# Optimization experiments

Measured on AMD Instinct MI355X. Metric: run time of the kernel, lower is better.

Reference implementation:

```python
import jax, jax.numpy as jnp
import numpy as np
import math

B, L, D, K = 8, 8192, 256, 2
J = math.ceil(math.log((L - 1) / (K - 1) + 1) / math.log(K))  # 13 for L=8192, K=2


def setup_inputs() -> dict:
    key = jax.random.key(0)
    kx, k0, k1, kw = jax.random.split(key, 4)
    # matches nn.initializers.normal(stddev=h_scale) in the flax module
    h_scale = math.sqrt((math.gamma(K / 2) / math.gamma(J + K / 2)) ** (1.0 / J) / 2.0)
    x = jax.random.normal(kx, (B, L, D), dtype=jnp.float32)
    h0 = jax.random.normal(k0, (D, K), dtype=jnp.float32) * h_scale
    h1 = jax.random.normal(k1, (D, K), dtype=jnp.float32) * h_scale
    w = jax.random.normal(kw, (J + 2, D), dtype=jnp.float32) / math.sqrt(J + 2)
    return {"x": x, "h0": h0, "h1": h1, "w": w}


def _depthwise_conv(a, filt, dilation, d):
    # a: (B, L', D), filt: (1, D, K) in IOL layout, depthwise via feature_group_count=D
    return jax.lax.conv_general_dilated(
        lhs=a, rhs=filt, window_strides=(1,), padding='VALID',
        dimension_numbers=('NLC', 'IOL', 'NLC'),
        rhs_dilation=(dilation,), feature_group_count=d)


def reference(x, h0, h1, w):
    Kf = h0.shape[-1]
    Dd = x.shape[-1]
    h0r = h0[None, :, :]  # (1, D, K)
    h1r = h1[None, :, :]
    Jlv = w.shape[0] - 2
    y = jnp.zeros_like(x)
    a = x
    for j in range(Jlv):
        dilation = Kf ** j
        pad = dilation * (Kf - 1)
        a = jnp.pad(a, ((0, 0), (pad, 0), (0, 0)))  # pad left (pad_right=False)
        b = _depthwise_conv(a, h1r, dilation, Dd)
        a = _depthwise_conv(a, h0r, dilation, Dd)
        y = y + w[j + 1][None, None, :] * b
    y = y + w[None, :1, :] * x + w[None, -1:, :] * a
    return y
```

## Files before the change

kernel.cpp:

```cpp
#include <hip/hip_runtime.h>
#include <hip/hip_bf16.h>
#include <stdint.h>

namespace {

constexpr int L = 8192;
constexpr int D = 256;

constexpr int K1_CT  = 32;
constexpr int K1_OUT = 192;
constexpr int K1_S   = 265;

constexpr int K2_CT = 32;
constexpr int K2_T2 = 2;
constexpr int K2_S  = 131;

__device__ __forceinline__ int phi1(int p) { return p + (p >> 5); }
__device__ __forceinline__ int phi2(int t) { return t + (t >> 5); }

__device__ __forceinline__ uint32_t pk2(float ylo, float ahi) {
    union { __hip_bfloat16 h; uint16_t u; } a, b;
    a.h = __float2bfloat16(ylo);
    b.h = __float2bfloat16(ahi);
    return ((uint32_t)b.u << 16) | (uint32_t)a.u;
}
__device__ __forceinline__ float up_lo(uint32_t u) { return __uint_as_float(u << 16); }
__device__ __forceinline__ float up_hi(uint32_t u) { return __uint_as_float(u & 0xffff0000u); }

__device__ __forceinline__ void lvl4(float (&a)[4], float (&y)[4],
                                     float l0, float l1, float l2, float l3,
                                     float h00, float h01, float h10, float h11,
                                     float wj) {
    const float lk[4] = {l0, l1, l2, l3};
#pragma unroll
    for (int i = 0; i < 4; ++i) {
        const float bv = lk[i] * h10 + a[i] * h11;
        y[i] = fmaf(wj, bv, y[i]);
        a[i] = lk[i] * h00 + a[i] * h01;
    }
}

__device__ __forceinline__ void lvl2f(float& a0, float& a1, float& y0, float& y1,
                                      float l0, float l1,
                                      float h00, float h01, float h10, float h11,
                                      float wj) {
    const float bv0 = l0 * h10 + a0 * h11;
    const float bv1 = l1 * h10 + a1 * h11;
    y0 = fmaf(wj, bv0, y0);
    y1 = fmaf(wj, bv1, y1);
    a0 = l0 * h00 + a0 * h01;
    a1 = l1 * h00 + a1 * h01;
}

__global__ __launch_bounds__(512, 8)
void mrl_k1(const float* __restrict__ x, const float* __restrict__ h0,
            const float* __restrict__ h1, const float* __restrict__ w,
            uint32_t* __restrict__ out_pk) {
    __shared__ uint32_t lds[K1_CT * K1_S];
    __shared__ float cf[11 * K1_CT];
    const int tid = threadIdx.x;
    const int b  = blockIdx.z;
    const int c0 = blockIdx.y * K1_CT;
    const int t0 = blockIdx.x * K1_OUT;
    const int tsb = t0 - 64;

    if (tid < 11 * K1_CT) {
        const int r = tid >> 5, i = tid & 31;
        float v;
        if (r < 7)       v = w[r * D + c0 + i];
        else if (r == 7) v = h0[2 * (c0 + i)];
        else if (r == 8) v = h0[2 * (c0 + i) + 1];
        else if (r == 9) v = h1[2 * (c0 + i)];
        else             v = h1[2 * (c0 + i) + 1];
        cf[tid] = v;
    }

    {
        const int cq = (tid & 7) * 4;
        const int tr = tid >> 3;
        const float* xb = x + (size_t)b * L * D + c0 + cq;
#pragma unroll
        for (int it = 0; it < 4; ++it) {
            const int p = it * 64 + tr;
            const int t = tsb + p;
            float4 v = make_float4(0.f, 0.f, 0.f, 0.f);
            if (t >= 0 && t < L) v = *reinterpret_cast<const float4*>(xb + (size_t)t * D);
            const int ph = phi1(p);
            lds[(cq + 0) * K1_S + ph] = __float_as_uint(v.x);
            lds[(cq + 1) * K1_S + ph] = __float_as_uint(v.y);
            lds[(cq + 2) * K1_S + ph] = __float_as_uint(v.z);
            lds[(cq + 3) * K1_S + ph] = __float_as_uint(v.w);
        }
    }
    __syncthreads();

    {
        const int lane = tid & 63;
        const int wv   = tid >> 6;
        const int p0   = 4 * lane;
#pragma unroll
        for (int q = 0; q < 4; ++q) {
            const int cl = wv + 8 * q;
            const float h00 = cf[7*K1_CT + cl], h01 = cf[8*K1_CT + cl];
            const float h10 = cf[9*K1_CT + cl], h11 = cf[10*K1_CT + cl];
            const int base = cl * K1_S;
            float a[4], y[4];
            {
                const float w0 = cf[cl];
#pragma unroll
                for (int i = 0; i < 4; ++i) {
                    a[i] = __uint_as_float(lds[base + phi1(p0 + i)]);
                    y[i] = w0 * a[i];
                }
            }
            lvl4(a, y, __shfl_up(a[3], 1), a[0], a[1], a[2],
                 h00, h01, h10, h11, cf[1*K1_CT + cl]);
            lvl4(a, y, __shfl_up(a[2], 1), __shfl_up(a[3], 1), a[0], a[1],
                 h00, h01, h10, h11, cf[2*K1_CT + cl]);
            lvl4(a, y, __shfl_up(a[0], 1), __shfl_up(a[1], 1),
                       __shfl_up(a[2], 1), __shfl_up(a[3], 1),
                 h00, h01, h10, h11, cf[3*K1_CT + cl]);
            lvl4(a, y, __shfl_up(a[0], 2), __shfl_up(a[1], 2),
                       __shfl_up(a[2], 2), __shfl_up(a[3], 2),
                 h00, h01, h10, h11, cf[4*K1_CT + cl]);
            lvl4(a, y, __shfl_up(a[0], 4), __shfl_up(a[1], 4),
                       __shfl_up(a[2], 4), __shfl_up(a[3], 4),
                 h00, h01, h10, h11, cf[5*K1_CT + cl]);
            lvl4(a, y, __shfl_up(a[0], 8), __shfl_up(a[1], 8),
                       __shfl_up(a[2], 8), __shfl_up(a[3], 8),
                 h00, h01, h10, h11, cf[6*K1_CT + cl]);
#pragma unroll
            for (int i = 0; i < 4; ++i)
                lds[base + phi1(p0 + i)] = pk2(y[i], a[i]);
        }
    }
    __syncthreads();

    {
        const int cq = (tid & 7) * 4;
        const int tr = tid >> 3;
        uint32_t* ob = out_pk + (size_t)b * L * D + c0 + cq;
#pragma unroll
        for (int it = 0; it < 3; ++it) {
            const int p = 64 + it * 64 + tr;
            const int t = tsb + p;
            if (t < L) {
                const int ph = phi1(p);
                uint4 v;
                v.x = lds[(cq + 0) * K1_S + ph];
                v.y = lds[(cq + 1) * K1_S + ph];
                v.z = lds[(cq + 2) * K1_S + ph];
                v.w = lds[(cq + 3) * K1_S + ph];
                *reinterpret_cast<uint4*>(ob + (size_t)t * D) = v;
            }
        }
    }
}

__global__ __launch_bounds__(512, 8)
void mrl_k2(const float* __restrict__ h0, const float* __restrict__ h1,
            const float* __restrict__ w, float* __restrict__ y) {
    __shared__ uint32_t lds[K2_CT * K2_T2 * K2_S];
    __shared__ float cf[12 * K2_CT];
    const int tid = threadIdx.x;
    const int b   = blockIdx.z;
    const int c0  = blockIdx.y * K2_CT;
    const int t2a = blockIdx.x * K2_T2;
    uint32_t* yb = reinterpret_cast<uint32_t*>(y) + (size_t)b * L * D + c0;

    if (tid < 12 * K2_CT) {
        const int r = tid >> 5, i = tid & 31;
        float v;
        if (r < 8)        v = w[(r + 7) * D + c0 + i];
        else if (r == 8)  v = h0[2 * (c0 + i)];
        else if (r == 9)  v = h0[2 * (c0 + i) + 1];
        else if (r == 10) v = h1[2 * (c0 + i)];
        else              v = h1[2 * (c0 + i) + 1];
        cf[tid] = v;
    }

    {
        const int cq  = (tid & 7) * 4;
        const int t2i = (tid >> 3) & 1;
        const int t1r = tid >> 4;
#pragma unroll
        for (int it = 0; it < 4; ++it) {
            const int t1 = it * 32 + t1r;
            const int t  = t1 * 64 + t2a + t2i;
            const uint4 v = *reinterpret_cast<const uint4*>(yb + (size_t)t * D + cq);
            const int ph = phi2(t1);
            lds[((cq + 0) * 2 + t2i) * K2_S + ph] = v.x;
            lds[((cq + 1) * 2 + t2i) * K2_S + ph] = v.y;
            lds[((cq + 2) * 2 + t2i) * K2_S + ph] = v.z;
            lds[((cq + 3) * 2 + t2i) * K2_S + ph] = v.w;
        }
    }
    __syncthreads();

    {
        const int lane = tid & 63;
        const int wv   = tid >> 6;
#pragma unroll
        for (int q = 0; q < 8; ++q) {
            const int pr = wv + 8 * q;
            const int cl = pr >> 1;
            const float h00 = cf[8*K2_CT + cl],  h01 = cf[9*K2_CT + cl];
            const float h10 = cf[10*K2_CT + cl], h11 = cf[11*K2_CT + cl];
            const int base = pr * K2_S;
            float a0, a1, y0, y1v;
            {
                const uint32_t u0 = lds[base + phi2(2 * lane)];
                const uint32_t u1 = lds[base + phi2(2 * lane + 1)];
                a0 = up_hi(u0); y0  = up_lo(u0);
                a1 = up_hi(u1); y1v = up_lo(u1);
            }
            {
                const float s = __shfl_up(a1, 1);
                const float l0 = (lane >= 1) ? s : 0.f;
                lvl2f(a0, a1, y0, y1v, l0, a0, h00, h01, h10, h11, cf[cl]);
            }
#pragma unroll
            for (int k = 0; k < 6; ++k) {
                const int m = 1 << k;
                const float wj = cf[(1 + k) * K2_CT + cl];
                const float s0 = __shfl_up(a0, m);
                const float s1 = __shfl_up(a1, m);
                const bool ok = (lane >= m);
                const float l0 = ok ? s0 : 0.f;
                const float l1 = ok ? s1 : 0.f;
                lvl2f(a0, a1, y0, y1v, l0, l1, h00, h01, h10, h11, wj);
            }
            const float w14 = cf[7 * K2_CT + cl];
            y0  = fmaf(w14, a0, y0);
            y1v = fmaf(w14, a1, y1v);
            lds[base + phi2(2 * lane)]     = __float_as_uint(y0);
            lds[base + phi2(2 * lane + 1)] = __float_as_uint(y1v);
        }
    }
    __syncthreads();

    {
        const int cq = (tid & 7) * 4;
        const int rq = tid >> 3;
#pragma unroll
        for (int it = 0; it < 4; ++it) {
            const int row = it * 64 + rq;
            const int t1 = row >> 1, t2i = row & 1;
            const int t  = t1 * 64 + t2a + t2i;
            const int ph = phi2(t1);
            uint4 v;
            v.x = lds[((cq + 0) * 2 + t2i) * K2_S + ph];
            v.y = lds[((cq + 1) * 2 + t2i) * K2_S + ph];
            v.z = lds[((cq + 2) * 2 + t2i) * K2_S + ph];
            v.w = lds[((cq + 3) * 2 + t2i) * K2_S + ph];
            *reinterpret_cast<uint4*>(yb + (size_t)t * D + cq) = v;
        }
    }
}

}

extern "C" void kernel_launch(void* const* d_in, const int* in_sizes, int n_in,
                              void* d_out, int out_size, void* d_ws, size_t ws_size,
                              hipStream_t stream) {
    const float* x  = (const float*)d_in[0];
    const float* h0 = (const float*)d_in[1];
    const float* h1 = (const float*)d_in[2];
    const float* w  = (const float*)d_in[3];
    float* y = (float*)d_out;
    (void)d_ws; (void)ws_size;

    const int B = in_sizes[0] / (L * D);

    dim3 g1((L + K1_OUT - 1) / K1_OUT, D / K1_CT, B);
    dim3 g2(64 / K2_T2, D / K2_CT, B);

    mrl_k1<<<g1, 512, 0, stream>>>(x, h0, h1, w, (uint32_t*)y);
    mrl_k2<<<g2, 512, 0, stream>>>(h0, h1, w, y);
}
```

Measured before the change: 164.7 us.

## Interleave channel chains, vectorize LDS accesses, load coefficients as scalars

Both kernels now process all of a wave's channels level by level instead of one channel at a time. The independent shuffle and FMA chains can then overlap and hide cross-lane latency. The LDS padding changes from one to two words per 32 elements, so each thread's 4 or 2 consecutive values can be read and written with 64-bit LDS accesses. The shared coefficient table and its staging are removed; filter and weight values are loaded directly from global memory using wave-uniform (readfirstlane) channel indices. The cost is higher register pressure from holding all per-channel state at once, which could limit occupancy or cause spills.

```diff
diff --git a/kernel.cpp b/kernel.cpp
--- a/kernel.cpp
+++ b/kernel.cpp
@@ -9,14 +9,13 @@
 
 constexpr int K1_CT  = 32;
 constexpr int K1_OUT = 192;
-constexpr int K1_S   = 265;
+constexpr int K1_S   = 270;
 
 constexpr int K2_CT = 32;
 constexpr int K2_T2 = 2;
-constexpr int K2_S  = 131;
-
-__device__ __forceinline__ int phi1(int p) { return p + (p >> 5); }
-__device__ __forceinline__ int phi2(int t) { return t + (t >> 5); }
+constexpr int K2_S  = 134;
+
+__device__ __forceinline__ int phie(int p) { return p + 2 * (p >> 5); }
 
 __device__ __forceinline__ uint32_t pk2(float ylo, float ahi) {
     union { __hip_bfloat16 h; uint16_t u; } a, b;
@@ -27,6 +26,12 @@
 __device__ __forceinline__ float up_lo(uint32_t u) { return __uint_as_float(u << 16); }
 __device__ __forceinline__ float up_hi(uint32_t u) { return __uint_as_float(u & 0xffff0000u); }
 
+__device__ __forceinline__ float sh1(float v) { return __shfl_up(v, 1); }
+__device__ __forceinline__ float sh1z(float v, int lane) {
+    const float s = __shfl_up(v, 1);
+    return (lane >= 1) ? s : 0.f;
+}
+
 __device__ __forceinline__ void lvl4(float (&a)[4], float (&y)[4],
                                      float l0, float l1, float l2, float l3,
                                      float h00, float h01, float h10, float h11,
@@ -40,41 +45,17 @@
     }
 }
 
-__device__ __forceinline__ void lvl2f(float& a0, float& a1, float& y0, float& y1,
-                                      float l0, float l1,
-                                      float h00, float h01, float h10, float h11,
-                                      float wj) {
-    const float bv0 = l0 * h10 + a0 * h11;
-    const float bv1 = l1 * h10 + a1 * h11;
-    y0 = fmaf(wj, bv0, y0);
-    y1 = fmaf(wj, bv1, y1);
-    a0 = l0 * h00 + a0 * h01;
-    a1 = l1 * h00 + a1 * h01;
-}
-
 __global__ __launch_bounds__(512, 8)
 void mrl_k1(const float* __restrict__ x, const float* __restrict__ h0,
             const float* __restrict__ h1, const float* __restrict__ w,
             uint32_t* __restrict__ out_pk) {
     __shared__ uint32_t lds[K1_CT * K1_S];
-    __shared__ float cf[11 * K1_CT];
     const int tid = threadIdx.x;
     const int b  = blockIdx.z;
     const int c0 = blockIdx.y * K1_CT;
     const int t0 = blockIdx.x * K1_OUT;
     const int tsb = t0 - 64;
 
-    if (tid < 11 * K1_CT) {
-        const int r = tid >> 5, i = tid & 31;
-        float v;
-        if (r < 7)       v = w[r * D + c0 + i];
-        else if (r == 7) v = h0[2 * (c0 + i)];
-        else if (r == 8) v = h0[2 * (c0 + i) + 1];
-        else if (r == 9) v = h1[2 * (c0 + i)];
-        else             v = h1[2 * (c0 + i) + 1];
-        cf[tid] = v;
-    }
-
     {
         const int cq = (tid & 7) * 4;
         const int tr = tid >> 3;
@@ -85,7 +66,7 @@
             const int t = tsb + p;
             float4 v = make_float4(0.f, 0.f, 0.f, 0.f);
             if (t >= 0 && t < L) v = *reinterpret_cast<const float4*>(xb + (size_t)t * D);
-            const int ph = phi1(p);
+            const int ph = phie(p);
             lds[(cq + 0) * K1_S + ph] = __float_as_uint(v.x);
             lds[(cq + 1) * K1_S + ph] = __float_as_uint(v.y);
             lds[(cq + 2) * K1_S + ph] = __float_as_uint(v.z);
@@ -97,41 +78,67 @@
     {
         const int lane = tid & 63;
         const int wv   = tid >> 6;
-        const int p0   = 4 * lane;
-#pragma unroll
-        for (int q = 0; q < 4; ++q) {
-            const int cl = wv + 8 * q;
-            const float h00 = cf[7*K1_CT + cl], h01 = cf[8*K1_CT + cl];
-            const float h10 = cf[9*K1_CT + cl], h11 = cf[10*K1_CT + cl];
-            const int base = cl * K1_S;
-            float a[4], y[4];
-            {
-                const float w0 = cf[cl];
-#pragma unroll
-                for (int i = 0; i < 4; ++i) {
-                    a[i] = __uint_as_float(lds[base + phi1(p0 + i)]);
-                    y[i] = w0 * a[i];
-                }
-            }
-            lvl4(a, y, __shfl_up(a[3], 1), a[0], a[1], a[2],
-                 h00, h01, h10, h11, cf[1*K1_CT + cl]);
-            lvl4(a, y, __shfl_up(a[2], 1), __shfl_up(a[3], 1), a[0], a[1],
-                 h00, h01, h10, h11, cf[2*K1_CT + cl]);
-            lvl4(a, y, __shfl_up(a[0], 1), __shfl_up(a[1], 1),
-                       __shfl_up(a[2], 1), __shfl_up(a[3], 1),
-                 h00, h01, h10, h11, cf[3*K1_CT + cl]);
-            lvl4(a, y, __shfl_up(a[0], 2), __shfl_up(a[1], 2),
-                       __shfl_up(a[2], 2), __shfl_up(a[3], 2),
-                 h00, h01, h10, h11, cf[4*K1_CT + cl]);
-            lvl4(a, y, __shfl_up(a[0], 4), __shfl_up(a[1], 4),
-                       __shfl_up(a[2], 4), __shfl_up(a[3], 4),
-                 h00, h01, h10, h11, cf[5*K1_CT + cl]);
-            lvl4(a, y, __shfl_up(a[0], 8), __shfl_up(a[1], 8),
-                       __shfl_up(a[2], 8), __shfl_up(a[3], 8),
-                 h00, h01, h10, h11, cf[6*K1_CT + cl]);
-#pragma unroll
-            for (int i = 0; i < 4; ++i)
-                lds[base + phi1(p0 + i)] = pk2(y[i], a[i]);
+        const int p0  = 4 * lane;
+        const int ph0 = phie(p0);
+
+        int cu[4];
+        float h00[4], h01[4], h10[4], h11[4];
+#pragma unroll
+        for (int u = 0; u < 4; ++u) {
+            cu[u] = __builtin_amdgcn_readfirstlane(c0 + wv + 8 * u);
+            h00[u] = h0[2 * cu[u]];  h01[u] = h0[2 * cu[u] + 1];
+            h10[u] = h1[2 * cu[u]];  h11[u] = h1[2 * cu[u] + 1];
+        }
+
+        float A[4][4], Y[4][4];
+#pragma unroll
+        for (int u = 0; u < 4; ++u) {
+            const int base = (wv + 8 * u) * K1_S + ph0;
+            const uint2 r0 = *reinterpret_cast<const uint2*>(&lds[base]);
+            const uint2 r1 = *reinterpret_cast<const uint2*>(&lds[base + 2]);
+            A[u][0] = __uint_as_float(r0.x); A[u][1] = __uint_as_float(r0.y);
+            A[u][2] = __uint_as_float(r1.x); A[u][3] = __uint_as_float(r1.y);
+            const float w0 = w[cu[u]];
+#pragma unroll
+            for (int i = 0; i < 4; ++i) Y[u][i] = w0 * A[u][i];
+        }
+
+#pragma unroll
+        for (int u = 0; u < 4; ++u)
+            lvl4(A[u], Y[u], sh1(A[u][3]), A[u][0], A[u][1], A[u][2],
+                 h00[u], h01[u], h10[u], h11[u], w[1 * D + cu[u]]);
+#pragma unroll
+        for (int u = 0; u < 4; ++u)
+            lvl4(A[u], Y[u], sh1(A[u][2]), sh1(A[u][3]), A[u][0], A[u][1],
+                 h00[u], h01[u], h10[u], h11[u], w[2 * D + cu[u]]);
+#pragma unroll
+        for (int u = 0; u < 4; ++u)
+            lvl4(A[u], Y[u], sh1(A[u][0]), sh1(A[u][1]), sh1(A[u][2]), sh1(A[u][3]),
+                 h00[u], h01[u], h10[u], h11[u], w[3 * D + cu[u]]);
+#pragma unroll
+        for (int u = 0; u < 4; ++u)
+            lvl4(A[u], Y[u], __shfl_up(A[u][0], 2), __shfl_up(A[u][1], 2),
+                 __shfl_up(A[u][2], 2), __shfl_up(A[u][3], 2),
+                 h00[u], h01[u], h10[u], h11[u], w[4 * D + cu[u]]);
+#pragma unroll
+        for (int u = 0; u < 4; ++u)
+            lvl4(A[u], Y[u], __shfl_up(A[u][0], 4), __shfl_up(A[u][1], 4),
+                 __shfl_up(A[u][2], 4), __shfl_up(A[u][3], 4),
+                 h00[u], h01[u], h10[u], h11[u], w[5 * D + cu[u]]);
+#pragma unroll
+        for (int u = 0; u < 4; ++u)
+            lvl4(A[u], Y[u], __shfl_up(A[u][0], 8), __shfl_up(A[u][1], 8),
+                 __shfl_up(A[u][2], 8), __shfl_up(A[u][3], 8),
+                 h00[u], h01[u], h10[u], h11[u], w[6 * D + cu[u]]);
+
+#pragma unroll
+        for (int u = 0; u < 4; ++u) {
+            const int base = (wv + 8 * u) * K1_S + ph0;
+            uint2 w0v, w1v;
+            w0v.x = pk2(Y[u][0], A[u][0]); w0v.y = pk2(Y[u][1], A[u][1]);
+            w1v.x = pk2(Y[u][2], A[u][2]); w1v.y = pk2(Y[u][3], A[u][3]);
+            *reinterpret_cast<uint2*>(&lds[base])     = w0v;
+            *reinterpret_cast<uint2*>(&lds[base + 2]) = w1v;
         }
     }
     __syncthreads();
@@ -145,7 +152,7 @@
             const int p = 64 + it * 64 + tr;
             const int t = tsb + p;
             if (t < L) {
-                const int ph = phi1(p);
+                const int ph = phie(p);
                 uint4 v;
                 v.x = lds[(cq + 0) * K1_S + ph];
                 v.y = lds[(cq + 1) * K1_S + ph];
@@ -161,24 +168,12 @@
 void mrl_k2(const float* __restrict__ h0, const float* __restrict__ h1,
             const float* __restrict__ w, float* __restrict__ y) {
     __shared__ uint32_t lds[K2_CT * K2_T2 * K2_S];
-    __shared__ float cf[12 * K2_CT];
     const int tid = threadIdx.x;
     const int b   = blockIdx.z;
     const int c0  = blockIdx.y * K2_CT;
     const int t2a = blockIdx.x * K2_T2;
     uint32_t* yb = reinterpret_cast<uint32_t*>(y) + (size_t)b * L * D + c0;
 
-    if (tid < 12 * K2_CT) {
-        const int r = tid >> 5, i = tid & 31;
-        float v;
-        if (r < 8)        v = w[(r + 7) * D + c0 + i];
-        else if (r == 8)  v = h0[2 * (c0 + i)];
-        else if (r == 9)  v = h0[2 * (c0 + i) + 1];
-        else if (r == 10) v = h1[2 * (c0 + i)];
-        else              v = h1[2 * (c0 + i) + 1];
-        cf[tid] = v;
-    }
-
     {
         const int cq  = (tid & 7) * 4;
         const int t2i = (tid >> 3) & 1;
@@ -188,7 +183,7 @@
             const int t1 = it * 32 + t1r;
             const int t  = t1 * 64 + t2a + t2i;
             const uint4 v = *reinterpret_cast<const uint4*>(yb + (size_t)t * D + cq);
-            const int ph = phi2(t1);
+            const int ph = phie(t1);
             lds[((cq + 0) * 2 + t2i) * K2_S + ph] = v.x;
             lds[((cq + 1) * 2 + t2i) * K2_S + ph] = v.y;
             lds[((cq + 2) * 2 + t2i) * K2_S + ph] = v.z;
@@ -200,41 +195,77 @@
     {
         const int lane = tid & 63;
         const int wv   = tid >> 6;
-#pragma unroll
-        for (int q = 0; q < 8; ++q) {
-            const int pr = wv + 8 * q;
-            const int cl = pr >> 1;
-            const float h00 = cf[8*K2_CT + cl],  h01 = cf[9*K2_CT + cl];
-            const float h10 = cf[10*K2_CT + cl], h11 = cf[11*K2_CT + cl];
-            const int base = pr * K2_S;
-            float a0, a1, y0, y1v;
-            {
-                const uint32_t u0 = lds[base + phi2(2 * lane)];
-                const uint32_t u1 = lds[base + phi2(2 * lane + 1)];
-                a0 = up_hi(u0); y0  = up_lo(u0);
-                a1 = up_hi(u1); y1v = up_lo(u1);
-            }
-            {
-                const float s = __shfl_up(a1, 1);
-                const float l0 = (lane >= 1) ? s : 0.f;
-                lvl2f(a0, a1, y0, y1v, l0, a0, h00, h01, h10, h11, cf[cl]);
-            }
-#pragma unroll
-            for (int k = 0; k < 6; ++k) {
-                const int m = 1 << k;
-                const float wj = cf[(1 + k) * K2_CT + cl];
-                const float s0 = __shfl_up(a0, m);
-                const float s1 = __shfl_up(a1, m);
+        const int ph0  = phie(2 * lane);
+
+        int cu[8];
+        float h00[8], h01[8], h10[8], h11[8];
+#pragma unroll
+        for (int q = 0; q < 8; ++q) {
+            cu[q] = __builtin_amdgcn_readfirstlane(c0 + ((wv + 8 * q) >> 1));
+            h00[q] = h0[2 * cu[q]];  h01[q] = h0[2 * cu[q] + 1];
+            h10[q] = h1[2 * cu[q]];  h11[q] = h1[2 * cu[q] + 1];
+        }
+
+        float A0[8], A1[8], Y0[8], Y1[8];
+#pragma unroll
+        for (int q = 0; q < 8; ++q) {
+            const int base = (wv + 8 * q) * K2_S + ph0;
+            const uint2 r = *reinterpret_cast<const uint2*>(&lds[base]);
+            A0[q] = up_hi(r.x); Y0[q] = up_lo(r.x);
+            A1[q] = up_hi(r.y); Y1[q] = up_lo(r.y);
+        }
+
+#pragma unroll
+        for (int q = 0; q < 8; ++q) {
+            const float wj = w[7 * D + cu[q]];
+            const float l0 = sh1z(A1[q], lane);
+            const float l1 = A0[q];
+            const float bv0 = l0 * h10[q] + A0[q] * h11[q];
+            const float bv1 = l1 * h10[q] + A1[q] * h11[q];
+            Y0[q] = fmaf(wj, bv0, Y0[q]);
+            Y1[q] = fmaf(wj, bv1, Y1[q]);
+            A0[q] = l0 * h00[q] + A0[q] * h01[q];
+            A1[q] = l1 * h00[q] + A1[q] * h01[q];
+        }
+#pragma unroll
+        for (int q = 0; q < 8; ++q) {
+            const float wj = w[8 * D + cu[q]];
+            const float l0 = sh1z(A0[q], lane);
+            const float l1 = sh1z(A1[q], lane);
+            const float bv0 = l0 * h10[q] + A0[q] * h11[q];
+            const float bv1 = l1 * h10[q] + A1[q] * h11[q];
+            Y0[q] = fmaf(wj, bv0, Y0[q]);
+            Y1[q] = fmaf(wj, bv1, Y1[q]);
+            A0[q] = l0 * h00[q] + A0[q] * h01[q];
+            A1[q] = l1 * h00[q] + A1[q] * h01[q];
+        }
+#pragma unroll
+        for (int k = 0; k < 5; ++k) {
+            const int m = 2 << k;
+#pragma unroll
+            for (int q = 0; q < 8; ++q) {
+                const float wj = w[(9 + k) * D + cu[q]];
+                const float s0 = __shfl_up(A0[q], m);
+                const float s1 = __shfl_up(A1[q], m);
                 const bool ok = (lane >= m);
                 const float l0 = ok ? s0 : 0.f;
                 const float l1 = ok ? s1 : 0.f;
-                lvl2f(a0, a1, y0, y1v, l0, l1, h00, h01, h10, h11, wj);
+                const float bv0 = l0 * h10[q] + A0[q] * h11[q];
+                const float bv1 = l1 * h10[q] + A1[q] * h11[q];
+                Y0[q] = fmaf(wj, bv0, Y0[q]);
+                Y1[q] = fmaf(wj, bv1, Y1[q]);
+                A0[q] = l0 * h00[q] + A0[q] * h01[q];
+                A1[q] = l1 * h00[q] + A1[q] * h01[q];
             }
-            const float w14 = cf[7 * K2_CT + cl];
-            y0  = fmaf(w14, a0, y0);
-            y1v = fmaf(w14, a1, y1v);
-            lds[base + phi2(2 * lane)]     = __float_as_uint(y0);
-            lds[base + phi2(2 * lane + 1)] = __float_as_uint(y1v);
+        }
+#pragma unroll
+        for (int q = 0; q < 8; ++q) {
+            const float w14 = w[14 * D + cu[q]];
+            const int base = (wv + 8 * q) * K2_S + ph0;
+            uint2 wv2;
+            wv2.x = __float_as_uint(fmaf(w14, A0[q], Y0[q]));
+            wv2.y = __float_as_uint(fmaf(w14, A1[q], Y1[q]));
+            *reinterpret_cast<uint2*>(&lds[base]) = wv2;
         }
     }
     __syncthreads();
@@ -247,7 +278,7 @@
             const int row = it * 64 + rq;
             const int t1 = row >> 1, t2i = row & 1;
             const int t  = t1 * 64 + t2a + t2i;
-            const int ph = phi2(t1);
+            const int ph = phie(t1);
             uint4 v;
             v.x = lds[((cq + 0) * 2 + t2i) * K2_S + ph];
             v.y = lds[((cq + 1) * 2 + t2i) * K2_S + ph];
```

Result: slower. 171.5 us (+4.1%).
